# Kernel tuning notes

Hardware: AMD Instinct MI355X
Metric: run time of the kernel (lower is better)

The kernel has to match this reference:

```python
import jax, jax.numpy as jnp
import numpy as np

B, IN, OUT, T = 64, 1024, 512, 512
V_TH = 1.0
TAU = 16.0


def alpha_kernel(t, tau):
    # SRM alpha kernel: (t/tau)*exp(1 - t/tau) for t > 0, else 0.
    # Mask BEFORE exp to avoid overflow for large negative t.
    ts = jnp.where(t > 0, t, tau)
    v = (ts / tau) * jnp.exp(1.0 - ts / tau)
    return jnp.where(t > 0, v, 0.0)


def setup_inputs() -> dict:
    key = jax.random.key(0)
    k1, k2 = jax.random.split(key)
    # input spike times in [0, T/2)
    in_spike = jax.random.uniform(k1, (B, IN), dtype=jnp.float32) * (T / 2)
    weight = jax.random.normal(k2, (OUT, IN), dtype=jnp.float32) / np.float32(np.sqrt(IN))
    return {"in_spike": in_spike, "weight": weight}


def reference(in_spike, weight):
    t_seq = jnp.arange(T, dtype=jnp.float32)                  # [T]
    time_sequence = t_seq[None, None, :] - in_spike[:, :, None]  # [B, in, T]
    v_input = alpha_kernel(time_sequence, TAU)                 # [B, in, T]
    # fc applied along the `in` axis at every time step
    membrane_voltage = jnp.einsum('bit,oi->bot', v_input, weight)  # [B, out, T]
    # first time index where voltage crosses threshold; T if never.
    mask = membrane_voltage >= V_TH                            # [B, out, T]
    spiked = mask.any(axis=-1)
    first_t = jnp.argmax(mask, axis=-1)                        # first True index
    out_spike = jnp.where(spiked, first_t, T).astype(jnp.float32)  # [B, out]
    return out_spike
```

## Files before the change

### kernel.cpp

```cpp
#include <hip/hip_runtime.h>
#include <math.h>

#define BATCH   64
#define INS     1024
#define OUTS    512
#define TSTEPS  512
#define TAUF    16.0f
#define LOG2E_OVER_TAU 0.0901684400555602f

#define TT 64
#define NTRANS ((INS / TT) * (OUTS / TT))

__global__ __launch_bounds__(256) void pre_kernel(
        const float* __restrict__ w, float* __restrict__ wT,
        const float* __restrict__ in_spike, float4* __restrict__ spk,
        int* __restrict__ starts) {
    __shared__ float tile[TT][TT + 1];
    __shared__ int hist[257];
    __shared__ int cursor[257];
    __shared__ int wsum[4];

    if (blockIdx.x < NTRANS) {
        const int i0 = (blockIdx.x & (INS / TT - 1)) * TT;
        const int o0 = (blockIdx.x / (INS / TT)) * TT;
        const int c  = threadIdx.x & 63;
        const int r  = threadIdx.x >> 6;
#pragma unroll
        for (int rr = r; rr < TT; rr += 4)
            tile[rr][c] = w[(o0 + rr) * INS + i0 + c];
        __syncthreads();
#pragma unroll
        for (int rr = r; rr < TT; rr += 4)
            wT[(i0 + rr) * OUTS + o0 + c] = tile[c][rr];
        return;
    }

    const int b = blockIdx.x - NTRANS;
    const int tid = threadIdx.x;
    for (int k = tid; k < 257; k += 256) hist[k] = 0;
    __syncthreads();

    float sv[INS / 256];
    int   tv[INS / 256];
#pragma unroll
    for (int j = 0; j < INS / 256; ++j) {
        int i = tid + j * 256;
        float s = in_spike[b * INS + i];
        sv[j] = s;
        int t = (int)floorf(s) + 1;
        t = t < 1 ? 1 : (t > 256 ? 256 : t);
        tv[j] = t;
        atomicAdd(&hist[t], 1);
    }
    __syncthreads();

    const int lane = tid & 63;
    const int wv   = tid >> 6;
    int v = hist[tid + 1];
    int sc = v;
#pragma unroll
    for (int off = 1; off < 64; off <<= 1) {
        int n = __shfl_up(sc, off, 64);
        if (lane >= off) sc += n;
    }
    if (lane == 63) wsum[wv] = sc;
    __syncthreads();
    int base = 0;
    for (int j = 0; j < wv; ++j) base += wsum[j];
    int excl = sc + base - v;
    cursor[tid + 1] = excl;
    starts[b * 258 + tid + 1] = excl;
    if (tid == 0) { starts[b * 258] = 0; starts[b * 258 + 257] = INS; }
    __syncthreads();

#pragma unroll
    for (int j = 0; j < INS / 256; ++j) {
        int i = tid + j * 256;
        int t = tv[j];
        int pos = atomicAdd(&cursor[t], 1);
        float A = expf(fmaf(sv[j], 1.0f / TAUF, 1.0f)) * (1.0f / TAUF);
        float C = -sv[j] * A;
        spk[b * INS + pos] =
            make_float4(A, __int_as_float(i * (OUTS / 2)), C, __int_as_float(t));
    }
}

#define OL 32
#define G  32
#define WS 8
#define TAIL0 257

__global__ __launch_bounds__(OL * G, 8) void spike_scan_kernel(
        const float4* __restrict__ spk, const int* __restrict__ starts,
        const float* __restrict__ wT, float* __restrict__ out) {
    const int b = blockIdx.x;
    const int x = threadIdx.x;
    const int g = threadIdx.y;
    const int tid = g * OL + x;

    __shared__ float4 sspk[INS];
    __shared__ float2 psP0[G][OL];
    __shared__ float2 psP1[G][OL];
    __shared__ int    sSt[258];
    __shared__ int    sFirst[2 * OL];

    sspk[tid] = spk[b * INS + tid];
    if (tid < 258) sSt[tid] = starts[b * 258 + tid];
    if (tid < 2 * OL) sFirst[tid] = TSTEPS;
    __syncthreads();

    const int w0 = g * WS + 1;
    const float2* __restrict__ wT2x = (const float2*)wT + (blockIdx.y * OL + x);

    float cA0 = 0.f, cC0 = 0.f, cA1 = 0.f, cC1 = 0.f;
    float l00, l01, l02, l03, l04, l05, l06, l07;
    float l10, l11, l12, l13, l14, l15, l16, l17;
    int k = sSt[w0];

#define BUCKET(D, LA, LB)                                                     \
    {                                                                         \
        const int e = sSt[w0 + (D) + 1];                                      \
        for (; k + 2 <= e; k += 2) {                                          \
            float4 p0 = sspk[k + 0];                                          \
            float4 p1 = sspk[k + 1];                                          \
            float2 q0 = wT2x[__float_as_int(p0.y)];                           \
            float2 q1 = wT2x[__float_as_int(p1.y)];                           \
            cA0 = fmaf(q0.x, p0.x, cA0); cC0 = fmaf(q0.x, p0.z, cC0);         \
            cA1 = fmaf(q0.y, p0.x, cA1); cC1 = fmaf(q0.y, p0.z, cC1);         \
            cA0 = fmaf(q1.x, p1.x, cA0); cC0 = fmaf(q1.x, p1.z, cC0);         \
            cA1 = fmaf(q1.y, p1.x, cA1); cC1 = fmaf(q1.y, p1.z, cC1);         \
        }                                                                     \
        if (k < e) {                                                          \
            float4 p = sspk[k];                                               \
            float2 q = wT2x[__float_as_int(p.y)];                             \
            cA0 = fmaf(q.x, p.x, cA0); cC0 = fmaf(q.x, p.z, cC0);             \
            cA1 = fmaf(q.y, p.x, cA1); cC1 = fmaf(q.y, p.z, cC1);             \
            ++k;                                                              \
        }                                                                     \
        const float tf = (float)(w0 + (D));                                   \
        LA = fmaf(tf, cA0, cC0);                                              \
        LB = fmaf(tf, cA1, cC1);                                              \
    }

    BUCKET(0, l00, l10)
    BUCKET(1, l01, l11)
    BUCKET(2, l02, l12)
    BUCKET(3, l03, l13)
    BUCKET(4, l04, l14)
    BUCKET(5, l05, l15)
    BUCKET(6, l06, l16)
    BUCKET(7, l07, l17)
#undef BUCKET

    psP0[g][x] = make_float2(cA0, cC0);
    psP1[g][x] = make_float2(cA1, cC1);
    __syncthreads();

    float SA0 = 0.f, SC0 = 0.f, SA1 = 0.f, SC1 = 0.f;
    for (int j = 0; j < g; ++j) {
        float2 a = psP0[j][x];
        float2 c = psP1[j][x];
        SA0 += a.x; SC0 += a.y; SA1 += c.x; SC1 += c.y;
    }
    float TA0 = SA0, TC0 = SC0, TA1 = SA1, TC1 = SC1;
    for (int j = g; j < G; ++j) {
        float2 a = psP0[j][x];
        float2 c = psP1[j][x];
        TA0 += a.x; TC0 += a.y; TA1 += c.x; TC1 += c.y;
    }

    unsigned m0 = 0, m1 = 0;
#define CHECK(D, LA, LB)                                                      \
    {                                                                         \
        const float tf = (float)(w0 + (D));                                   \
        const float ev = exp2f(tf * LOG2E_OVER_TAU);                          \
        m0 |= (fmaf(tf, SA0, SC0) + (LA) >= ev) ? (1u << (D)) : 0u;           \
        m1 |= (fmaf(tf, SA1, SC1) + (LB) >= ev) ? (1u << (D)) : 0u;           \
    }
    CHECK(0, l00, l10)
    CHECK(1, l01, l11)
    CHECK(2, l02, l12)
    CHECK(3, l03, l13)
    CHECK(4, l04, l14)
    CHECK(5, l05, l15)
    CHECK(6, l06, l16)
    CHECK(7, l07, l17)
#undef CHECK
    int f0 = m0 ? (w0 + __builtin_ffs(m0) - 1) : TSTEPS;
    int f1 = m1 ? (w0 + __builtin_ffs(m1) - 1) : TSTEPS;

    {
        const int t0 = TAIL0 + g * WS;
        unsigned n0 = 0, n1 = 0;
        float tg = (float)t0;
        for (int d = 0; d < WS; ++d) {
            if (t0 + d < TSTEPS) {
                float ev = exp2f(tg * LOG2E_OVER_TAU);
                n0 |= (fmaf(tg, TA0, TC0) >= ev) ? (1u << d) : 0u;
                n1 |= (fmaf(tg, TA1, TC1) >= ev) ? (1u << d) : 0u;
            }
            tg += 1.0f;
        }
        if (n0) f0 = min(f0, t0 + __builtin_ffs(n0) - 1);
        if (n1) f1 = min(f1, t0 + __builtin_ffs(n1) - 1);
    }

    if (f0 < TSTEPS) atomicMin(&sFirst[2 * x], f0);
    if (f1 < TSTEPS) atomicMin(&sFirst[2 * x + 1], f1);
    __syncthreads();
    if (tid < 2 * OL)
        out[b * OUTS + blockIdx.y * (2 * OL) + tid] = (float)sFirst[tid];
}

extern "C" void kernel_launch(void* const* d_in, const int* in_sizes, int n_in,
                              void* d_out, int out_size, void* d_ws, size_t ws_size,
                              hipStream_t stream) {
    const float* in_spike = (const float*)d_in[0];
    const float* weight   = (const float*)d_in[1];
    float* out = (float*)d_out;

    float*  wT     = (float*)d_ws;
    float4* spk    = (float4*)((char*)d_ws + (size_t)INS * OUTS * sizeof(float));
    int*    starts = (int*)((char*)d_ws + (size_t)INS * OUTS * sizeof(float)
                                        + (size_t)BATCH * INS * sizeof(float4));

    pre_kernel<<<NTRANS + BATCH, 256, 0, stream>>>(weight, wT, in_spike, spk, starts);
    spike_scan_kernel<<<dim3(BATCH, OUTS / (2 * OL)), dim3(OL, G), 0, stream>>>(
        spk, starts, wT, out);
}
```

Baseline: 81.51 us.

## Narrow output tile, deepen time split, and use log-step prefix scan

```diff
diff --git a/kernel.cpp b/kernel.cpp
--- a/kernel.cpp
+++ b/kernel.cpp
@@ -85,9 +85,9 @@
     }
 }
 
-#define OL 32
-#define G  32
-#define WS 8
+#define OL 16
+#define G  64
+#define WS 4
 #define TAIL0 257
 
 __global__ __launch_bounds__(OL * G, 8) void spike_scan_kernel(
@@ -99,8 +99,7 @@
     const int tid = g * OL + x;
 
     __shared__ float4 sspk[INS];
-    __shared__ float2 psP0[G][OL];
-    __shared__ float2 psP1[G][OL];
+    __shared__ float4 sscan[2][G][OL];
     __shared__ int    sSt[258];
     __shared__ int    sFirst[2 * OL];
 
@@ -113,8 +112,8 @@
     const float2* __restrict__ wT2x = (const float2*)wT + (blockIdx.y * OL + x);
 
     float cA0 = 0.f, cC0 = 0.f, cA1 = 0.f, cC1 = 0.f;
-    float l00, l01, l02, l03, l04, l05, l06, l07;
-    float l10, l11, l12, l13, l14, l15, l16, l17;
+    float l00, l01, l02, l03;
+    float l10, l11, l12, l13;
     int k = sSt[w0];
 
 #define BUCKET(D, LA, LB)                                                     \
@@ -146,28 +145,26 @@
     BUCKET(1, l01, l11)
     BUCKET(2, l02, l12)
     BUCKET(3, l03, l13)
-    BUCKET(4, l04, l14)
-    BUCKET(5, l05, l15)
-    BUCKET(6, l06, l16)
-    BUCKET(7, l07, l17)
 #undef BUCKET
 
-    psP0[g][x] = make_float2(cA0, cC0);
-    psP1[g][x] = make_float2(cA1, cC1);
-    __syncthreads();
-
-    float SA0 = 0.f, SC0 = 0.f, SA1 = 0.f, SC1 = 0.f;
-    for (int j = 0; j < g; ++j) {
-        float2 a = psP0[j][x];
-        float2 c = psP1[j][x];
-        SA0 += a.x; SC0 += a.y; SA1 += c.x; SC1 += c.y;
-    }
-    float TA0 = SA0, TC0 = SC0, TA1 = SA1, TC1 = SC1;
-    for (int j = g; j < G; ++j) {
-        float2 a = psP0[j][x];
-        float2 c = psP1[j][x];
-        TA0 += a.x; TC0 += a.y; TA1 += c.x; TC1 += c.y;
-    }
+    const float4 own = make_float4(cA0, cC0, cA1, cC1);
+    sscan[0][g][x] = own;
+    __syncthreads();
+
+    float4 cur = own;
+    int p = 0;
+    for (int off = 1; off < G; off <<= 1) {
+        float4 t = (g >= off) ? sscan[p][g - off][x]
+                              : make_float4(0.f, 0.f, 0.f, 0.f);
+        cur.x += t.x; cur.y += t.y; cur.z += t.z; cur.w += t.w;
+        sscan[p ^ 1][g][x] = cur;
+        __syncthreads();
+        p ^= 1;
+    }
+    const float SA0 = cur.x - own.x, SC0 = cur.y - own.y;
+    const float SA1 = cur.z - own.z, SC1 = cur.w - own.w;
+    const float4 tot = sscan[p][G - 1][x];
+    const float TA0 = tot.x, TC0 = tot.y, TA1 = tot.z, TC1 = tot.w;
 
     unsigned m0 = 0, m1 = 0;
 #define CHECK(D, LA, LB)                                                      \
@@ -181,10 +178,6 @@
     CHECK(1, l01, l11)
     CHECK(2, l02, l12)
     CHECK(3, l03, l13)
-    CHECK(4, l04, l14)
-    CHECK(5, l05, l15)
-    CHECK(6, l06, l16)
-    CHECK(7, l07, l17)
 #undef CHECK
     int f0 = m0 ? (w0 + __builtin_ffs(m0) - 1) : TSTEPS;
     int f1 = m1 ? (w0 + __builtin_ffs(m1) - 1) : TSTEPS;
```

New measurement: 84.92 us. 4.2% more time.

## Fuse per-batch spike bucket sort into the scan kernel

Applied to the files above, without the earlier changes.

```diff
diff --git a/kernel.cpp b/kernel.cpp
--- a/kernel.cpp
+++ b/kernel.cpp
@@ -12,77 +12,19 @@
 #define NTRANS ((INS / TT) * (OUTS / TT))
 
 __global__ __launch_bounds__(256) void pre_kernel(
-        const float* __restrict__ w, float* __restrict__ wT,
-        const float* __restrict__ in_spike, float4* __restrict__ spk,
-        int* __restrict__ starts) {
+        const float* __restrict__ w, float* __restrict__ wT) {
     __shared__ float tile[TT][TT + 1];
-    __shared__ int hist[257];
-    __shared__ int cursor[257];
-    __shared__ int wsum[4];
-
-    if (blockIdx.x < NTRANS) {
-        const int i0 = (blockIdx.x & (INS / TT - 1)) * TT;
-        const int o0 = (blockIdx.x / (INS / TT)) * TT;
-        const int c  = threadIdx.x & 63;
-        const int r  = threadIdx.x >> 6;
+    const int i0 = (blockIdx.x & (INS / TT - 1)) * TT;
+    const int o0 = (blockIdx.x / (INS / TT)) * TT;
+    const int c  = threadIdx.x & 63;
+    const int r  = threadIdx.x >> 6;
 #pragma unroll
-        for (int rr = r; rr < TT; rr += 4)
-            tile[rr][c] = w[(o0 + rr) * INS + i0 + c];
-        __syncthreads();
+    for (int rr = r; rr < TT; rr += 4)
+        tile[rr][c] = w[(o0 + rr) * INS + i0 + c];
+    __syncthreads();
 #pragma unroll
-        for (int rr = r; rr < TT; rr += 4)
-            wT[(i0 + rr) * OUTS + o0 + c] = tile[c][rr];
-        return;
-    }
-
-    const int b = blockIdx.x - NTRANS;
-    const int tid = threadIdx.x;
-    for (int k = tid; k < 257; k += 256) hist[k] = 0;
-    __syncthreads();
-
-    float sv[INS / 256];
-    int   tv[INS / 256];
-#pragma unroll
-    for (int j = 0; j < INS / 256; ++j) {
-        int i = tid + j * 256;
-        float s = in_spike[b * INS + i];
-        sv[j] = s;
-        int t = (int)floorf(s) + 1;
-        t = t < 1 ? 1 : (t > 256 ? 256 : t);
-        tv[j] = t;
-        atomicAdd(&hist[t], 1);
-    }
-    __syncthreads();
-
-    const int lane = tid & 63;
-    const int wv   = tid >> 6;
-    int v = hist[tid + 1];
-    int sc = v;
-#pragma unroll
-    for (int off = 1; off < 64; off <<= 1) {
-        int n = __shfl_up(sc, off, 64);
-        if (lane >= off) sc += n;
-    }
-    if (lane == 63) wsum[wv] = sc;
-    __syncthreads();
-    int base = 0;
-    for (int j = 0; j < wv; ++j) base += wsum[j];
-    int excl = sc + base - v;
-    cursor[tid + 1] = excl;
-    starts[b * 258 + tid + 1] = excl;
-    if (tid == 0) { starts[b * 258] = 0; starts[b * 258 + 257] = INS; }
-    __syncthreads();
-
-#pragma unroll
-    for (int j = 0; j < INS / 256; ++j) {
-        int i = tid + j * 256;
-        int t = tv[j];
-        int pos = atomicAdd(&cursor[t], 1);
-        float A = expf(fmaf(sv[j], 1.0f / TAUF, 1.0f)) * (1.0f / TAUF);
-        float C = -sv[j] * A;
-        spk[b * INS + pos] =
-            make_float4(A, __int_as_float(i * (OUTS / 2)), C, __int_as_float(t));
-    }
+    for (int rr = r; rr < TT; rr += 4)
+        wT[(i0 + rr) * OUTS + o0 + c] = tile[c][rr];
 }
 
 #define OL 32
@@ -91,8 +33,8 @@
 #define TAIL0 257
 
 __global__ __launch_bounds__(OL * G, 8) void spike_scan_kernel(
-        const float4* __restrict__ spk, const int* __restrict__ starts,
-        const float* __restrict__ wT, float* __restrict__ out) {
+        const float* __restrict__ in_spike, const float* __restrict__ wT,
+        float* __restrict__ out) {
     const int b = blockIdx.x;
     const int x = threadIdx.x;
     const int g = threadIdx.y;
@@ -101,12 +43,49 @@
     __shared__ float4 sspk[INS];
     __shared__ float2 psP0[G][OL];
     __shared__ float2 psP1[G][OL];
+    __shared__ int    hist[257];
+    __shared__ int    cursor[257];
     __shared__ int    sSt[258];
+    __shared__ int    wsum[4];
     __shared__ int    sFirst[2 * OL];
 
-    sspk[tid] = spk[b * INS + tid];
-    if (tid < 258) sSt[tid] = starts[b * 258 + tid];
+    if (tid < 257) hist[tid] = 0;
     if (tid < 2 * OL) sFirst[tid] = TSTEPS;
+    float s = in_spike[b * INS + tid];
+    int t = (int)floorf(s) + 1;
+    t = t < 1 ? 1 : (t > 256 ? 256 : t);
+    float A = expf(fmaf(s, 1.0f / TAUF, 1.0f)) * (1.0f / TAUF);
+    float C = -s * A;
+    __syncthreads();
+    atomicAdd(&hist[t], 1);
+    __syncthreads();
+
+    int sc = 0;
+    if (tid < 256) {
+        int v = hist[tid + 1];
+        sc = v;
+#pragma unroll
+        for (int off = 1; off < 64; off <<= 1) {
+            int n = __shfl_up(sc, off, 64);
+            if ((tid & 63) >= off) sc += n;
+        }
+        if ((tid & 63) == 63) wsum[tid >> 6] = sc;
+    }
+    __syncthreads();
+    if (tid < 256) {
+        int base = 0;
+        for (int j = 0; j < (tid >> 6); ++j) base += wsum[j];
+        int excl = sc + base - hist[tid + 1];
+        sSt[tid + 1] = excl;
+        cursor[tid + 1] = excl;
+        if (tid == 0) { sSt[0] = 0; sSt[257] = INS; }
+    }
+    __syncthreads();
+    {
+        int pos = atomicAdd(&cursor[t], 1);
+        sspk[pos] = make_float4(A, __int_as_float(tid * (OUTS / 2)),
+                                C, __int_as_float(t));
+    }
     __syncthreads();
 
     const int w0 = g * WS + 1;
@@ -219,12 +198,9 @@
     const float* weight   = (const float*)d_in[1];
     float* out = (float*)d_out;
 
-    float*  wT     = (float*)d_ws;
-    float4* spk    = (float4*)((char*)d_ws + (size_t)INS * OUTS * sizeof(float));
-    int*    starts = (int*)((char*)d_ws + (size_t)INS * OUTS * sizeof(float)
-                                        + (size_t)BATCH * INS * sizeof(float4));
-
-    pre_kernel<<<NTRANS + BATCH, 256, 0, stream>>>(weight, wT, in_spike, spk, starts);
+    float* wT = (float*)d_ws;
+
+    pre_kernel<<<NTRANS, 256, 0, stream>>>(weight, wT);
     spike_scan_kernel<<<dim3(BATCH, OUTS / (2 * OL)), dim3(OL, G), 0, stream>>>(
-        spk, starts, wT, out);
+        in_spike, wT, out);
 }
```

Measured after the change: 84.03 us. 3.1% more time.
